# Optimization experiments

Measured on AMD Instinct MI355X. Metric: run time of the kernel, lower is better.

Reference implementation:

```python
import jax, jax.numpy as jnp
import numpy as np

B, T, C, H = 4, 2048, 1024, 16
HS = C // H  # head_size = 64


def setup_inputs() -> dict:
    key = jax.random.key(0)
    ks = jax.random.split(key, 12)
    s_in = C ** -0.5
    s_ff = (4 * C) ** -0.5
    return {
        "x": jax.random.normal(ks[0], (B, T, C), jnp.float32),
        "Wq": jax.random.normal(ks[1], (H, C, HS), jnp.float32) * s_in,
        "Wk": jax.random.normal(ks[2], (H, C, HS), jnp.float32) * s_in,
        "Wv": jax.random.normal(ks[3], (H, C, HS), jnp.float32) * s_in,
        "Wp": jax.random.normal(ks[4], (C, C), jnp.float32) * s_in,
        "bp": jnp.zeros((C,), jnp.float32),
        "W1": jax.random.normal(ks[5], (C, 4 * C), jnp.float32) * s_in,
        "b1": jnp.zeros((4 * C,), jnp.float32),
        "W2": jax.random.normal(ks[6], (4 * C, C), jnp.float32) * s_ff,
        "b2": jnp.zeros((C,), jnp.float32),
        "g1": jnp.ones((C,), jnp.float32),
        "be1": jnp.zeros((C,), jnp.float32),
        "g2": jnp.ones((C,), jnp.float32),
        "be2": jnp.zeros((C,), jnp.float32),
    }


def _layernorm(x, g, b, eps=1e-5):
    mu = jnp.mean(x, axis=-1, keepdims=True)
    var = jnp.var(x, axis=-1, keepdims=True)
    return (x - mu) * jax.lax.rsqrt(var + eps) * g + b


def reference(x, Wq, Wk, Wv, Wp, bp, W1, b1, W2, b2, g1, be1, g2, be2):
    # NOTE: residuals add to the post-LN tensor (faithful to the torch code),
    # and the attention scale uses C = n_embed, not head_size.
    x1 = _layernorm(x, g1, be1)                       # [B,T,C]
    q = jnp.einsum('btc,hcd->bhtd', x1, Wq)
    k = jnp.einsum('btc,hcd->bhtd', x1, Wk)
    v = jnp.einsum('btc,hcd->bhtd', x1, Wv)
    scores = jnp.einsum('bhtd,bhsd->bhts', q, k) * (C ** -0.5)
    causal = jnp.tril(jnp.ones((T, T), bool))
    scores = jnp.where(causal, scores, -jnp.inf)
    att = jax.nn.softmax(scores, axis=-1)             # [B,H,T,T]
    o = jnp.einsum('bhts,bhsd->bhtd', att, v)
    o = o.transpose(0, 2, 1, 3).reshape(B, T, C)      # concat heads
    x2 = x1 + o @ Wp + bp
    x3 = _layernorm(x2, g2, be2)
    ff = jax.nn.relu(x3 @ W1 + b1) @ W2 + b2
    return x3 + ff
```

## Files before the change

### kernel.cpp

```cpp
#include <hip/hip_runtime.h>
#include <cstdint>

typedef unsigned short u16;
typedef unsigned int u32;
typedef __bf16 bf16x8 __attribute__((ext_vector_type(8)));
typedef float f32x4 __attribute__((ext_vector_type(4)));

#define DEVINL __device__ __forceinline__

DEVINL float bf2f(u16 h) { union { u32 u; float f; } v; v.u = ((u32)h) << 16; return v.f; }
DEVINL u16 f2bf(float f) {
  union { float f; u32 u; } v; v.f = f;
  u32 u = v.u;
  return (u16)((u + 0x7fffu + ((u >> 16) & 1u)) >> 16);
}

DEVINL void gld_lds16(const void* g, void* l) {
  __builtin_amdgcn_global_load_lds(
      (__attribute__((address_space(1))) void*)(g),
      (__attribute__((address_space(3))) void*)(l), 16, 0, 0);
}

__global__ __launch_bounds__(256) void ktransf(const float* __restrict__ in,
                                               u16* __restrict__ out,
                                               int R, int C, long ibs, long obs) {
  __shared__ __align__(16) u16 tile[64][80];
  const float* ip = in + (long)blockIdx.z * ibs;
  u16* op = out + (long)blockIdx.z * obs;
  int c0 = blockIdx.x * 64, r0 = blockIdx.y * 64;
  int t = threadIdx.x;
#pragma unroll
  for (int ph = 0; ph < 2; ++ph) {
    int ch = ph * 256 + t;
    int r = ch >> 3, cc = (ch & 7) * 8;
    const float* src = &ip[(long)(r0 + r) * C + c0 + cc];
    float4 a = *(const float4*)src;
    float4 b = *(const float4*)(src + 4);
    u16 tmp[8] = {f2bf(a.x), f2bf(a.y), f2bf(a.z), f2bf(a.w),
                  f2bf(b.x), f2bf(b.y), f2bf(b.z), f2bf(b.w)};
    *(uint4*)&tile[r][cc] = *(uint4*)tmp;
  }
  __syncthreads();
#pragma unroll
  for (int ph = 0; ph < 2; ++ph) {
    int ch = ph * 256 + t;
    int c = ch >> 3, rr = (ch & 7) * 8;
    u16 tmp[8];
#pragma unroll
    for (int i = 0; i < 8; ++i) tmp[i] = tile[rr + i][c];
    *(uint4*)&op[(long)(c0 + c) * R + r0 + rr] = *(uint4*)tmp;
  }
}

__global__ __launch_bounds__(256) void ktransb(const u16* __restrict__ in,
                                               u16* __restrict__ out,
                                               int R, int C, long ibs, long obs) {
  __shared__ __align__(16) u16 tile[64][80];
  const u16* ip = in + (long)blockIdx.z * ibs;
  u16* op = out + (long)blockIdx.z * obs;
  int c0 = blockIdx.x * 64, r0 = blockIdx.y * 64;
  int t = threadIdx.x;
#pragma unroll
  for (int ph = 0; ph < 2; ++ph) {
    int ch = ph * 256 + t;
    int r = ch >> 3, cc = (ch & 7) * 8;
    *(uint4*)&tile[r][cc] = *(const uint4*)&ip[(long)(r0 + r) * C + c0 + cc];
  }
  __syncthreads();
#pragma unroll
  for (int ph = 0; ph < 2; ++ph) {
    int ch = ph * 256 + t;
    int c = ch >> 3, rr = (ch & 7) * 8;
    u16 tmp[8];
#pragma unroll
    for (int i = 0; i < 8; ++i) tmp[i] = tile[rr + i][c];
    *(uint4*)&op[(long)(c0 + c) * R + r0 + rr] = *(uint4*)tmp;
  }
}

__global__ __launch_bounds__(256) void kln_f(const float* __restrict__ x,
                                             const float* __restrict__ g,
                                             const float* __restrict__ be,
                                             u16* __restrict__ y) {
  long row = blockIdx.x;
  int t = threadIdx.x;
  float4 xv = *(const float4*)&x[row * 1024 + t * 4];
  float f0 = xv.x, f1 = xv.y, f2 = xv.z, f3 = xv.w;
  float s = f0 + f1 + f2 + f3;
  float s2 = f0 * f0 + f1 * f1 + f2 * f2 + f3 * f3;
#pragma unroll
  for (int off = 32; off >= 1; off >>= 1) {
    s += __shfl_xor(s, off);
    s2 += __shfl_xor(s2, off);
  }
  __shared__ float red[8];
  int w = t >> 6, l = t & 63;
  if (l == 0) { red[w] = s; red[4 + w] = s2; }
  __syncthreads();
  s = red[0] + red[1] + red[2] + red[3];
  s2 = red[4] + red[5] + red[6] + red[7];
  float mu = s * (1.0f / 1024.0f);
  float var = s2 * (1.0f / 1024.0f) - mu * mu;
  float rs = rsqrtf(var + 1e-5f);
  float4 gv = *(const float4*)&g[t * 4];
  float4 bv = *(const float4*)&be[t * 4];
  ushort4 ov;
  ov.x = f2bf((f0 - mu) * rs * gv.x + bv.x);
  ov.y = f2bf((f1 - mu) * rs * gv.y + bv.y);
  ov.z = f2bf((f2 - mu) * rs * gv.z + bv.z);
  ov.w = f2bf((f3 - mu) * rs * gv.w + bv.w);
  *(ushort4*)&y[row * 1024 + t * 4] = ov;
}

__global__ __launch_bounds__(256) void kln_b(const u16* __restrict__ x,
                                             const float* __restrict__ g,
                                             const float* __restrict__ be,
                                             u16* __restrict__ y) {
  long row = blockIdx.x;
  int t = threadIdx.x;
  ushort4 xv = *(const ushort4*)&x[row * 1024 + t * 4];
  float f0 = bf2f(xv.x), f1 = bf2f(xv.y), f2 = bf2f(xv.z), f3 = bf2f(xv.w);
  float s = f0 + f1 + f2 + f3;
  float s2 = f0 * f0 + f1 * f1 + f2 * f2 + f3 * f3;
#pragma unroll
  for (int off = 32; off >= 1; off >>= 1) {
    s += __shfl_xor(s, off);
    s2 += __shfl_xor(s2, off);
  }
  __shared__ float red[8];
  int w = t >> 6, l = t & 63;
  if (l == 0) { red[w] = s; red[4 + w] = s2; }
  __syncthreads();
  s = red[0] + red[1] + red[2] + red[3];
  s2 = red[4] + red[5] + red[6] + red[7];
  float mu = s * (1.0f / 1024.0f);
  float var = s2 * (1.0f / 1024.0f) - mu * mu;
  float rs = rsqrtf(var + 1e-5f);
  float4 gv = *(const float4*)&g[t * 4];
  float4 bv = *(const float4*)&be[t * 4];
  ushort4 ov;
  ov.x = f2bf((f0 - mu) * rs * gv.x + bv.x);
  ov.y = f2bf((f1 - mu) * rs * gv.y + bv.y);
  ov.z = f2bf((f2 - mu) * rs * gv.z + bv.z);
  ov.w = f2bf((f3 - mu) * rs * gv.w + bv.w);
  *(ushort4*)&y[row * 1024 + t * 4] = ov;
}

template <int EPI, int OF32>
__global__ __launch_bounds__(256) void kgemm(const u16* __restrict__ A,
                                             const u16* __restrict__ BT, int K,
                                             const float* __restrict__ bias,
                                             const u16* __restrict__ resid,
                                             void* __restrict__ outv, int ldc) {
  __shared__ __align__(16) u16 sA[128 * 64];
  __shared__ __align__(16) u16 sB[128 * 64];
  int tid = threadIdx.x;
  int l = tid & 63, wv = tid >> 6;
  int wm = (wv >> 1) * 64, wn = (wv & 1) * 64;
  long m0 = (long)blockIdx.y * 128, n0 = (long)blockIdx.x * 128;
  const u16* Ab = A + m0 * K;
  const u16* Bb = BT + n0 * K;
  f32x4 acc[4][4] = {};

  for (int k0 = 0; k0 < K; k0 += 64) {
    __syncthreads();
#pragma unroll
    for (int it = 0; it < 4; ++it) {
      int c = it * 256 + tid;
      int r = c >> 3;
      int k8 = (c & 7) ^ (r & 7);
      gld_lds16(Ab + (long)r * K + k0 + k8 * 8, &sA[c * 8]);
    }
#pragma unroll
    for (int it = 0; it < 4; ++it) {
      int c = it * 256 + tid;
      int r = c >> 3;
      int k8 = (c & 7) ^ (r & 7);
      gld_lds16(Bb + (long)r * K + k0 + k8 * 8, &sB[c * 8]);
    }
    __syncthreads();
#pragma unroll
    for (int kk = 0; kk < 2; ++kk) {
      int k8 = kk * 4 + (l >> 4);
      bf16x8 af[4], bfr[4];
#pragma unroll
      for (int mi = 0; mi < 4; ++mi) {
        int r = wm + mi * 16 + (l & 15);
        af[mi] = *(const bf16x8*)&sA[(r * 8 + (k8 ^ (r & 7))) * 8];
      }
#pragma unroll
      for (int ni = 0; ni < 4; ++ni) {
        int r = wn + ni * 16 + (l & 15);
        bfr[ni] = *(const bf16x8*)&sB[(r * 8 + (k8 ^ (r & 7))) * 8];
      }
#pragma unroll
      for (int mi = 0; mi < 4; ++mi)
#pragma unroll
        for (int ni = 0; ni < 4; ++ni)
          acc[mi][ni] =
              __builtin_amdgcn_mfma_f32_16x16x32_bf16(af[mi], bfr[ni], acc[mi][ni], 0, 0, 0);
    }
  }
#pragma unroll
  for (int mi = 0; mi < 4; ++mi) {
#pragma unroll
    for (int ni = 0; ni < 4; ++ni) {
#pragma unroll
      for (int j = 0; j < 4; ++j) {
        long row = m0 + wm + mi * 16 + (l >> 4) * 4 + j;
        long col = n0 + wn + ni * 16 + (l & 15);
        float v = acc[mi][ni][j];
        if constexpr (EPI == 0) {
          long tn = col >> 10, jj = col & 1023;
          long hh = jj >> 6, dd = jj & 63;
          long bb = row >> 11, tt = row & 2047;
          ((u16*)outv)[(((tn * 4 + bb) * 16 + hh) * 2048 + tt) * 64 + dd] = f2bf(v);
        } else {
          v += bias[col];
          if constexpr (EPI == 2) v = fmaxf(v, 0.0f);
          if constexpr (EPI == 1) v += bf2f(resid[row * ldc + col]);
          if constexpr (OF32) ((float*)outv)[row * ldc + col] = v;
          else ((u16*)outv)[row * ldc + col] = f2bf(v);
        }
      }
    }
  }
}

__global__ __launch_bounds__(256) void kattn(const u16* __restrict__ q,
                                             const u16* __restrict__ kmat,
                                             const u16* __restrict__ vt,
                                             u16* __restrict__ o) {
  __shared__ __align__(16) u16 Ks[64 * 64];
  __shared__ __align__(16) u16 Vs[64 * 64];
  __shared__ __align__(16) u16 Ps[4 * 32 * 64];
  int bh = blockIdx.x;
  int qi = (gridDim.y - 1) - blockIdx.y;
  int tid = threadIdx.x, w = tid >> 6, l = tid & 63;
  long bQ = (long)bh * 2048 * 64;
  int qrow0 = qi * 128 + w * 32;
  const float NEGINF = -__builtin_inff();

  bf16x8 qf[2][2];
#pragma unroll
  for (int mi = 0; mi < 2; ++mi)
#pragma unroll
    for (int kk = 0; kk < 2; ++kk) {
      int tt = qrow0 + mi * 16 + (l & 15);
      int kd = kk * 32 + (l >> 4) * 8;
      qf[mi][kk] = *(const bf16x8*)&q[bQ + (long)tt * 64 + kd];
    }
  f32x4 ao[2][4] = {};
  float mr[2][4], lr[2][4];
#pragma unroll
  for (int mi = 0; mi < 2; ++mi)
#pragma unroll
    for (int j = 0; j < 4; ++j) { mr[mi][j] = NEGINF; lr[mi][j] = 0.f; }

  u16* Pw = &Ps[w * 2048];
  int njt = qi * 2 + 2;
  for (int jt = 0; jt < njt; ++jt) {
    int s0 = jt * 64;
    __syncthreads();
#pragma unroll
    for (int it = 0; it < 2; ++it) {
      int c = it * 256 + tid;
      int r = c >> 3;
      int k8 = (c & 7) ^ (r & 7);
      gld_lds16(&kmat[bQ + (long)(s0 + r) * 64 + k8 * 8], &Ks[c * 8]);
    }
#pragma unroll
    for (int it = 0; it < 2; ++it) {
      int c = it * 256 + tid;
      int r = c >> 3;
      int s8 = (c & 7) ^ (r & 7);
      gld_lds16(&vt[bQ + (long)r * 2048 + s0 + s8 * 8], &Vs[c * 8]);
    }
    __syncthreads();
    f32x4 sc[2][4] = {};
#pragma unroll
    for (int kk = 0; kk < 2; ++kk) {
      int k8 = kk * 4 + (l >> 4);
      bf16x8 kf[4];
#pragma unroll
      for (int ni = 0; ni < 4; ++ni) {
        int r = ni * 16 + (l & 15);
        kf[ni] = *(const bf16x8*)&Ks[(r * 8 + (k8 ^ (r & 7))) * 8];
      }
#pragma unroll
      for (int mi = 0; mi < 2; ++mi)
#pragma unroll
        for (int ni = 0; ni < 4; ++ni)
          sc[mi][ni] =
              __builtin_amdgcn_mfma_f32_16x16x32_bf16(qf[mi][kk], kf[ni], sc[mi][ni], 0, 0, 0);
    }
#pragma unroll
    for (int mi = 0; mi < 2; ++mi) {
#pragma unroll
      for (int j = 0; j < 4; ++j) {
        int tg = qrow0 + mi * 16 + (l >> 4) * 4 + j;
        float rmax = NEGINF;
#pragma unroll
        for (int ni = 0; ni < 4; ++ni) {
          int sg = s0 + ni * 16 + (l & 15);
          float vv = sc[mi][ni][j] * 0.03125f;
          vv = (sg <= tg) ? vv : NEGINF;
          sc[mi][ni][j] = vv;
          rmax = fmaxf(rmax, vv);
        }
#pragma unroll
        for (int off = 8; off >= 1; off >>= 1) rmax = fmaxf(rmax, __shfl_xor(rmax, off));
        float mnew = fmaxf(mr[mi][j], rmax);
        float alpha = __expf(mr[mi][j] - mnew);
        float rsum = 0.f;
#pragma unroll
        for (int ni = 0; ni < 4; ++ni) {
          float p = __expf(sc[mi][ni][j] - mnew);
          sc[mi][ni][j] = p;
          rsum += p;
        }
#pragma unroll
        for (int off = 8; off >= 1; off >>= 1) rsum += __shfl_xor(rsum, off);
        lr[mi][j] = lr[mi][j] * alpha + rsum;
        mr[mi][j] = mnew;
#pragma unroll
        for (int nd = 0; nd < 4; ++nd) ao[mi][nd][j] *= alpha;
      }
    }
#pragma unroll
    for (int mi = 0; mi < 2; ++mi)
#pragma unroll
      for (int ni = 0; ni < 4; ++ni)
#pragma unroll
        for (int j = 0; j < 4; ++j) {
          int r = mi * 16 + (l >> 4) * 4 + j;
          int cc = ni * 16 + (l & 15);
          Pw[(r * 8 + ((cc >> 3) ^ (r & 7))) * 8 + (cc & 7)] = f2bf(sc[mi][ni][j]);
        }
#pragma unroll
    for (int kk = 0; kk < 2; ++kk) {
      int s8 = kk * 4 + (l >> 4);
      bf16x8 pf[2], vf[4];
#pragma unroll
      for (int mi = 0; mi < 2; ++mi) {
        int r = mi * 16 + (l & 15);
        pf[mi] = *(const bf16x8*)&Pw[(r * 8 + (s8 ^ (r & 7))) * 8];
      }
#pragma unroll
      for (int nd = 0; nd < 4; ++nd) {
        int r = nd * 16 + (l & 15);
        vf[nd] = *(const bf16x8*)&Vs[(r * 8 + (s8 ^ (r & 7))) * 8];
      }
#pragma unroll
      for (int mi = 0; mi < 2; ++mi)
#pragma unroll
        for (int nd = 0; nd < 4; ++nd)
          ao[mi][nd] =
              __builtin_amdgcn_mfma_f32_16x16x32_bf16(pf[mi], vf[nd], ao[mi][nd], 0, 0, 0);
    }
  }
  int b = bh >> 4, h = bh & 15;
#pragma unroll
  for (int mi = 0; mi < 2; ++mi)
#pragma unroll
    for (int nd = 0; nd < 4; ++nd)
#pragma unroll
      for (int j = 0; j < 4; ++j) {
        int tt = qrow0 + mi * 16 + (l >> 4) * 4 + j;
        int dd = nd * 16 + (l & 15);
        float v = ao[mi][nd][j] / lr[mi][j];
        o[((long)(b * 2048 + tt)) * 1024 + h * 64 + dd] = f2bf(v);
      }
}

extern "C" void kernel_launch(void* const* d_in, const int* in_sizes, int n_in,
                              void* d_out, int out_size, void* d_ws, size_t ws_size,
                              hipStream_t stream) {
  const float* x = (const float*)d_in[0];
  const float* Wq = (const float*)d_in[1];
  const float* Wk = (const float*)d_in[2];
  const float* Wv = (const float*)d_in[3];
  const float* Wp = (const float*)d_in[4];
  const float* bp = (const float*)d_in[5];
  const float* W1 = (const float*)d_in[6];
  const float* b1 = (const float*)d_in[7];
  const float* W2 = (const float*)d_in[8];
  const float* b2 = (const float*)d_in[9];
  const float* g1 = (const float*)d_in[10];
  const float* be1 = (const float*)d_in[11];
  const float* g2 = (const float*)d_in[12];
  const float* be2 = (const float*)d_in[13];

  u16* ws = (u16*)d_ws;
  u16* wqkvT = ws;
  u16* wpT = wqkvT + 3145728;
  u16* w1T = wpT + 1048576;
  u16* w2T = w1T + 4194304;
  u16* qb = w2T + 4194304;
  u16* kb = qb + 8388608;
  u16* vb = kb + 8388608;
  u16* vtb = vb + 8388608;
  u16* ob = vtb + 8388608;
  u16* x1 = ob + 8388608;
  float* outp = (float*)d_out;
  u16* x2 = vb;
  u16* x3 = ob;
  u16* hb = qb;

  ktransf<<<dim3(1, 16, 16), 256, 0, stream>>>(Wq, wqkvT, 1024, 64, 65536, 65536);
  ktransf<<<dim3(1, 16, 16), 256, 0, stream>>>(Wk, wqkvT + 1048576, 1024, 64, 65536, 65536);
  ktransf<<<dim3(1, 16, 16), 256, 0, stream>>>(Wv, wqkvT + 2097152, 1024, 64, 65536, 65536);
  ktransf<<<dim3(16, 16, 1), 256, 0, stream>>>(Wp, wpT, 1024, 1024, 0, 0);
  ktransf<<<dim3(64, 16, 1), 256, 0, stream>>>(W1, w1T, 1024, 4096, 0, 0);
  ktransf<<<dim3(16, 64, 1), 256, 0, stream>>>(W2, w2T, 4096, 1024, 0, 0);

  kln_f<<<8192, 256, 0, stream>>>(x, g1, be1, x1);
  kgemm<0, 0><<<dim3(24, 64), 256, 0, stream>>>(x1, wqkvT, 1024, nullptr, nullptr, qb, 0);
  ktransb<<<dim3(1, 32, 64), 256, 0, stream>>>(vb, vtb, 2048, 64, 131072, 131072);
  kattn<<<dim3(64, 16), 256, 0, stream>>>(qb, kb, vtb, ob);
  kgemm<1, 0><<<dim3(8, 64), 256, 0, stream>>>(ob, wpT, 1024, bp, x1, x2, 1024);
  kln_b<<<8192, 256, 0, stream>>>(x2, g2, be2, x3);
  kgemm<2, 0><<<dim3(32, 64), 256, 0, stream>>>(x3, w1T, 1024, b1, nullptr, hb, 4096);
  kgemm<1, 1><<<dim3(8, 64), 256, 0, stream>>>(hb, w2T, 4096, b2, x3, outp, 1024);
}
```

Baseline: 471.2 us.

## Fold softmax scale into Q projection, use exp2, widen attention KV tile

```diff
diff --git a/kernel.cpp b/kernel.cpp
--- a/kernel.cpp
+++ b/kernel.cpp
@@ -13,6 +13,14 @@
   union { float f; u32 u; } v; v.f = f;
   u32 u = v.u;
   return (u16)((u + 0x7fffu + ((u >> 16) & 1u)) >> 16);
+}
+
+DEVINL float fexp2(float x) {
+#if __has_builtin(__builtin_amdgcn_exp2f)
+  return __builtin_amdgcn_exp2f(x);
+#else
+  return exp2f(x);
+#endif
 }
 
 DEVINL void gld_lds16(const void* g, void* l) {
@@ -214,6 +222,7 @@
           long tn = col >> 10, jj = col & 1023;
           long hh = jj >> 6, dd = jj & 63;
           long bb = row >> 11, tt = row & 2047;
+          if (tn == 0) v *= 0.045084220027780106f;
           ((u16*)outv)[(((tn * 4 + bb) * 16 + hh) * 2048 + tt) * 64 + dd] = f2bf(v);
         } else {
           v += bias[col];
@@ -231,9 +240,9 @@
                                              const u16* __restrict__ kmat,
                                              const u16* __restrict__ vt,
                                              u16* __restrict__ o) {
-  __shared__ __align__(16) u16 Ks[64 * 64];
-  __shared__ __align__(16) u16 Vs[64 * 64];
-  __shared__ __align__(16) u16 Ps[4 * 32 * 64];
+  __shared__ __align__(16) u16 Ks[128 * 64];
+  __shared__ __align__(16) u16 Vs[64 * 128];
+  __shared__ __align__(16) u16 Ps[4 * 32 * 128];
   int bh = blockIdx.x;
   int qi = (gridDim.y - 1) - blockIdx.y;
   int tid = threadIdx.x, w = tid >> 6, l = tid & 63;
@@ -257,42 +266,46 @@
 #pragma unroll
     for (int j = 0; j < 4; ++j) { mr[mi][j] = NEGINF; lr[mi][j] = 0.f; }
 
-  u16* Pw = &Ps[w * 2048];
-  int njt = qi * 2 + 2;
+  u16* Pw = &Ps[w * 4096];
+  int njt = qi + 1;
   for (int jt = 0; jt < njt; ++jt) {
-    int s0 = jt * 64;
+    int s0 = jt * 128;
+    bool diag = (jt == njt - 1);
     __syncthreads();
 #pragma unroll
-    for (int it = 0; it < 2; ++it) {
+    for (int it = 0; it < 4; ++it) {
       int c = it * 256 + tid;
       int r = c >> 3;
       int k8 = (c & 7) ^ (r & 7);
       gld_lds16(&kmat[bQ + (long)(s0 + r) * 64 + k8 * 8], &Ks[c * 8]);
     }
 #pragma unroll
-    for (int it = 0; it < 2; ++it) {
+    for (int it = 0; it < 4; ++it) {
       int c = it * 256 + tid;
-      int r = c >> 3;
-      int s8 = (c & 7) ^ (r & 7);
+      int r = c >> 4;
+      int s8 = (c & 15) ^ (r & 7);
       gld_lds16(&vt[bQ + (long)r * 2048 + s0 + s8 * 8], &Vs[c * 8]);
     }
     __syncthreads();
-    f32x4 sc[2][4] = {};
+    f32x4 sc[2][8] = {};
 #pragma unroll
     for (int kk = 0; kk < 2; ++kk) {
       int k8 = kk * 4 + (l >> 4);
-      bf16x8 kf[4];
-#pragma unroll
-      for (int ni = 0; ni < 4; ++ni) {
-        int r = ni * 16 + (l & 15);
-        kf[ni] = *(const bf16x8*)&Ks[(r * 8 + (k8 ^ (r & 7))) * 8];
-      }
-#pragma unroll
-      for (int mi = 0; mi < 2; ++mi)
-#pragma unroll
-        for (int ni = 0; ni < 4; ++ni)
-          sc[mi][ni] =
-              __builtin_amdgcn_mfma_f32_16x16x32_bf16(qf[mi][kk], kf[ni], sc[mi][ni], 0, 0, 0);
+#pragma unroll
+      for (int nh = 0; nh < 2; ++nh) {
+        bf16x8 kf[4];
+#pragma unroll
+        for (int nn = 0; nn < 4; ++nn) {
+          int r = (nh * 4 + nn) * 16 + (l & 15);
+          kf[nn] = *(const bf16x8*)&Ks[(r * 8 + (k8 ^ (r & 7))) * 8];
+        }
+#pragma unroll
+        for (int mi = 0; mi < 2; ++mi)
+#pragma unroll
+          for (int nn = 0; nn < 4; ++nn)
+            sc[mi][nh * 4 + nn] = __builtin_amdgcn_mfma_f32_16x16x32_bf16(
+                qf[mi][kk], kf[nn], sc[mi][nh * 4 + nn], 0, 0, 0);
+      }
     }
 #pragma unroll
     for (int mi = 0; mi < 2; ++mi) {
@@ -300,22 +313,27 @@
       for (int j = 0; j < 4; ++j) {
         int tg = qrow0 + mi * 16 + (l >> 4) * 4 + j;
         float rmax = NEGINF;
-#pragma unroll
-        for (int ni = 0; ni < 4; ++ni) {
-          int sg = s0 + ni * 16 + (l & 15);
-          float vv = sc[mi][ni][j] * 0.03125f;
-          vv = (sg <= tg) ? vv : NEGINF;
-          sc[mi][ni][j] = vv;
-          rmax = fmaxf(rmax, vv);
+        if (diag) {
+#pragma unroll
+          for (int ni = 0; ni < 8; ++ni) {
+            int sg = s0 + ni * 16 + (l & 15);
+            float vv = sc[mi][ni][j];
+            vv = (sg <= tg) ? vv : NEGINF;
+            sc[mi][ni][j] = vv;
+            rmax = fmaxf(rmax, vv);
+          }
+        } else {
+#pragma unroll
+          for (int ni = 0; ni < 8; ++ni) rmax = fmaxf(rmax, sc[mi][ni][j]);
         }
 #pragma unroll
         for (int off = 8; off >= 1; off >>= 1) rmax = fmaxf(rmax, __shfl_xor(rmax, off));
         float mnew = fmaxf(mr[mi][j], rmax);
-        float alpha = __expf(mr[mi][j] - mnew);
+        float alpha = fexp2(mr[mi][j] - mnew);
         float rsum = 0.f;
 #pragma unroll
-        for (int ni = 0; ni < 4; ++ni) {
-          float p = __expf(sc[mi][ni][j] - mnew);
+        for (int ni = 0; ni < 8; ++ni) {
+          float p = fexp2(sc[mi][ni][j] - mnew);
           sc[mi][ni][j] = p;
           rsum += p;
         }
@@ -330,26 +348,26 @@
 #pragma unroll
     for (int mi = 0; mi < 2; ++mi)
 #pragma unroll
-      for (int ni = 0; ni < 4; ++ni)
+      for (int ni = 0; ni < 8; ++ni)
 #pragma unroll
         for (int j = 0; j < 4; ++j) {
           int r = mi * 16 + (l >> 4) * 4 + j;
           int cc = ni * 16 + (l & 15);
-          Pw[(r * 8 + ((cc >> 3) ^ (r & 7))) * 8 + (cc & 7)] = f2bf(sc[mi][ni][j]);
+          Pw[(r * 16 + ((cc >> 3) ^ (r & 7))) * 8 + (cc & 7)] = f2bf(sc[mi][ni][j]);
         }
 #pragma unroll
-    for (int kk = 0; kk < 2; ++kk) {
+    for (int kk = 0; kk < 4; ++kk) {
       int s8 = kk * 4 + (l >> 4);
       bf16x8 pf[2], vf[4];
 #pragma unroll
       for (int mi = 0; mi < 2; ++mi) {
         int r = mi * 16 + (l & 15);
-        pf[mi] = *(const bf16x8*)&Pw[(r * 8 + (s8 ^ (r & 7))) * 8];
+        pf[mi] = *(const bf16x8*)&Pw[(r * 16 + (s8 ^ (r & 7))) * 8];
       }
 #pragma unroll
       for (int nd = 0; nd < 4; ++nd) {
         int r = nd * 16 + (l & 15);
-        vf[nd] = *(const bf16x8*)&Vs[(r * 8 + (s8 ^ (r & 7))) * 8];
+        vf[nd] = *(const bf16x8*)&Vs[(r * 16 + (s8 ^ (r & 7))) * 8];
       }
 #pragma unroll
       for (int mi = 0; mi < 2; ++mi)
```

After: 510.3 us. 8.3% more time.
